# Kernel optimization log

Measured on AMD Instinct MI355X. Metric: run time of the kernel, lower is better.

## Reference

```python
import jax, jax.numpy as jnp
import numpy as np

B, S, HID = 2, 2048, 2048
NH, NKV, HD = 8, 2, 256
EPS = 1e-6
ROPE_THETA = 1e6


def _rms_norm(x, w):
    # Gemma3nRMSNorm: computed in fp32, x / sqrt(mean(x^2) + eps) * w
    xf = x.astype(jnp.float32)
    out = xf * jax.lax.rsqrt(jnp.mean(xf * xf, axis=-1, keepdims=True) + EPS) * w
    return out.astype(x.dtype)


def _rotate_half(x):
    x1, x2 = jnp.split(x, 2, axis=-1)
    return jnp.concatenate((-x2, x1), axis=-1)


def _apply_rope(x, cos, sin):
    # x: [B, S, H, D]; cos/sin: [B, S, D] -> unsqueeze head dim (unsqueeze_dim=2)
    c = cos[:, :, None, :]
    s = sin[:, :, None, :]
    return x * c + _rotate_half(x) * s


def setup_inputs() -> dict:
    key = jax.random.key(0)
    ks = jax.random.split(key, 6)
    hidden_states = jax.random.normal(ks[0], (B, S, HID), dtype=jnp.float32)
    # RoPE tables (theta = 1e6, Gemma3n)
    inv_freq = 1.0 / (ROPE_THETA ** (np.arange(0, HD, 2, dtype=np.float32) / HD))
    pos = np.arange(S, dtype=np.float32)
    freqs = pos[:, None] * inv_freq[None, :]            # [S, D/2]
    emb = np.concatenate([freqs, freqs], axis=-1)        # [S, D]
    cos = jnp.broadcast_to(jnp.asarray(np.cos(emb)), (B, S, HD)).astype(jnp.float32)
    sin = jnp.broadcast_to(jnp.asarray(np.sin(emb)), (B, S, HD)).astype(jnp.float32)
    # additive causal mask [B, 1, S, S]
    causal = jnp.tril(jnp.ones((S, S), dtype=bool))
    attention_mask = jnp.where(causal, 0.0, -1e9).astype(jnp.float32)
    attention_mask = jnp.broadcast_to(attention_mask[None, None], (B, 1, S, S))
    std = 0.02
    Wq = jax.random.normal(ks[1], (NH * HD, HID), dtype=jnp.float32) * std
    Wk = jax.random.normal(ks[2], (NKV * HD, HID), dtype=jnp.float32) * std
    Wv = jax.random.normal(ks[3], (NKV * HD, HID), dtype=jnp.float32) * std
    Wo = jax.random.normal(ks[4], (HID, NH * HD), dtype=jnp.float32) * std
    q_norm_w = jnp.ones((HD,), dtype=jnp.float32)
    k_norm_w = jnp.ones((HD,), dtype=jnp.float32)
    return {
        "hidden_states": hidden_states, "cos": cos, "sin": sin,
        "attention_mask": attention_mask,
        "Wq": Wq, "Wk": Wk, "Wv": Wv, "Wo": Wo,
        "q_norm_w": q_norm_w, "k_norm_w": k_norm_w,
    }


def reference(hidden_states, cos, sin, attention_mask, Wq, Wk, Wv, Wo, q_norm_w, k_norm_w):
    b, s, _ = hidden_states.shape
    # projections (no bias)
    q = (hidden_states @ Wq.T).reshape(b, s, NH, HD)
    k = (hidden_states @ Wk.T).reshape(b, s, NKV, HD)
    v = (hidden_states @ Wv.T).reshape(b, s, NKV, HD)
    # QK-norm then RoPE; v_norm has no scale (weight = 1)
    q = _apply_rope(_rms_norm(q, q_norm_w), cos, sin)
    k = _apply_rope(_rms_norm(k, k_norm_w), cos, sin)
    v = _rms_norm(v, jnp.float32(1.0))
    q = q.transpose(0, 2, 1, 3)  # [B, NH, S, D]
    k = k.transpose(0, 2, 1, 3)  # [B, NKV, S, D]
    v = v.transpose(0, 2, 1, 3)
    # repeat_kv: NKV -> NH (n_rep = NH // NKV)
    n_rep = NH // NKV
    k = jnp.repeat(k, n_rep, axis=1)
    v = jnp.repeat(v, n_rep, axis=1)
    # eager attention, scaling = 1.0 (as in Gemma3nTextAttention), no softcap
    scores = jnp.einsum("bhqd,bhkd->bhqk", q, k) + attention_mask
    probs = jax.nn.softmax(scores.astype(jnp.float32), axis=-1).astype(q.dtype)
    out = jnp.einsum("bhqk,bhkd->bqhd", probs, v).reshape(b, s, NH * HD)
    return out @ Wo.T
```

## Files before the change

kernel.cpp:

```cpp
#include <hip/hip_runtime.h>
#include <hip/hip_bf16.h>
#include <stdint.h>

#define S_LEN 2048
#define HIDN  2048
#define NH    8
#define NKV   2
#define HD    256

typedef _Float16 v8h __attribute__((ext_vector_type(8)));
typedef float    v4f __attribute__((ext_vector_type(4)));
typedef unsigned short u16;

struct alignas(8) US4 { u16 x, y, z, w; };

__device__ __forceinline__ u16 f2h(float f) {
  union { _Float16 h; u16 u; } t; t.h = (_Float16)f; return t.u;
}
__device__ __forceinline__ float h2f(u16 u) {
  union { _Float16 h; u16 u; } t; t.u = u; return (float)t.h;
}

template <typename T>
__device__ __forceinline__ void gload16(const T* g, void* l) {
  __builtin_amdgcn_global_load_lds(
      (const __attribute__((address_space(1))) void*)g,
      (__attribute__((address_space(3))) void*)l, 16, 0, 0);
}

__global__ void cvt_h_kernel(const float* __restrict__ in, u16* __restrict__ out, int n4) {
  int i = blockIdx.x * blockDim.x + threadIdx.x;
  if (i >= n4) return;
  float4 v = reinterpret_cast<const float4*>(in)[i];
  US4 o; o.x = f2h(v.x); o.y = f2h(v.y); o.z = f2h(v.z); o.w = f2h(v.w);
  reinterpret_cast<US4*>(out)[i] = o;
}

__global__ __launch_bounds__(256, 2) void gemm_h_nt(
    const u16* __restrict__ A, const u16* __restrict__ Bm,
    float* __restrict__ C, int M, int N, int K) {
  __shared__ u16 As[128 * 32];
  __shared__ u16 Bs[128 * 32];
  const int tid = threadIdx.x;
  const int w = tid >> 6, lane = tid & 63;
  const int m0 = blockIdx.x * 128, n0 = blockIdx.y * 128;
  const int wr = (w >> 1) * 64, wc = (w & 1) * 64;
  const int lr = lane & 15, lk = (lane >> 4) << 3;
  v4f acc[4][4] = {};
  const int row1 = tid >> 2, col1 = (tid & 3) << 3;
  const int t2 = tid + 256;
  const int row2 = t2 >> 2, col2 = (t2 & 3) << 3;
  for (int kt = 0; kt < K; kt += 32) {
    __syncthreads();
    gload16(A  + (size_t)(m0 + row1) * K + kt + col1, (char*)As + tid * 16);
    gload16(Bm + (size_t)(n0 + row1) * K + kt + col1, (char*)Bs + tid * 16);
    gload16(A  + (size_t)(m0 + row2) * K + kt + col2, (char*)As + t2 * 16);
    gload16(Bm + (size_t)(n0 + row2) * K + kt + col2, (char*)Bs + t2 * 16);
    __syncthreads();
    v8h af[4], bfr[4];
#pragma unroll
    for (int i = 0; i < 4; i++) af[i]  = *reinterpret_cast<const v8h*>(&As[(wr + i * 16 + lr) * 32 + lk]);
#pragma unroll
    for (int i = 0; i < 4; i++) bfr[i] = *reinterpret_cast<const v8h*>(&Bs[(wc + i * 16 + lr) * 32 + lk]);
#pragma unroll
    for (int i = 0; i < 4; i++)
#pragma unroll
      for (int jn = 0; jn < 4; jn++)
        acc[i][jn] = __builtin_amdgcn_mfma_f32_16x16x32_f16(af[i], bfr[jn], acc[i][jn], 0, 0, 0);
  }
  const int rbase = m0 + wr + ((lane >> 4) << 2);
  const int cbase = n0 + wc + lr;
#pragma unroll
  for (int i = 0; i < 4; i++)
#pragma unroll
    for (int jn = 0; jn < 4; jn++) {
      const int col = cbase + jn * 16;
#pragma unroll
      for (int j = 0; j < 4; j++)
        C[(size_t)(rbase + i * 16 + j) * N + col] = acc[i][jn][j];
    }
}

__global__ __launch_bounds__(256, 4) void norm_rope_kernel(
    const float* __restrict__ qkv, const float* __restrict__ cosb, const float* __restrict__ sinb,
    const float* __restrict__ qw, const float* __restrict__ kw,
    u16* __restrict__ q_t, u16* __restrict__ k_t, u16* __restrict__ v_t) {
  const int task = blockIdx.x * 4 + (threadIdx.x >> 6);
  const int lane = threadIdx.x & 63;
  const int unit = task % 12;
  const int ms = task / 12;
  const int b = ms >> 11, s = ms & 2047;
  const int d0 = lane << 2;
  const int col0 = (unit < 8) ? unit * 256 : 2048 + (unit - 8) * 256;
  const float4 xv = *reinterpret_cast<const float4*>(qkv + (size_t)ms * 3072 + col0 + d0);
  float x[4] = { xv.x, xv.y, xv.z, xv.w };
  float ss = x[0]*x[0] + x[1]*x[1] + x[2]*x[2] + x[3]*x[3];
#pragma unroll
  for (int m = 1; m < 64; m <<= 1) ss += __shfl_xor(ss, m, 64);
  const float r = rsqrtf(ss * (1.0f / 256.0f) + 1e-6f);
  if (unit < 10) {
    const float4 wv = *reinterpret_cast<const float4*>(((unit < 8) ? qw : kw) + d0);
    float xn[4];
    xn[0] = x[0] * r * wv.x; xn[1] = x[1] * r * wv.y;
    xn[2] = x[2] * r * wv.z; xn[3] = x[3] * r * wv.w;
    float rot[4];
#pragma unroll
    for (int j = 0; j < 4; j++) {
      const float p = __shfl(xn[j], lane ^ 32, 64);
      rot[j] = (lane < 32) ? -p : p;
    }
    const float4 c  = *reinterpret_cast<const float4*>(cosb + (size_t)ms * 256 + d0);
    const float4 sn = *reinterpret_cast<const float4*>(sinb + (size_t)ms * 256 + d0);
    US4 o;
    o.x = f2h(xn[0] * c.x + rot[0] * sn.x);
    o.y = f2h(xn[1] * c.y + rot[1] * sn.y);
    o.z = f2h(xn[2] * c.z + rot[2] * sn.z);
    o.w = f2h(xn[3] * c.w + rot[3] * sn.w);
    if (unit < 8) {
      const size_t dst = ((size_t)(b * NH + unit) * S_LEN + s) * 256 + d0;
      *reinterpret_cast<US4*>(q_t + dst) = o;
    } else {
      const size_t dst = ((size_t)(b * NKV + (unit - 8)) * S_LEN + s) * 256 + d0;
      *reinterpret_cast<US4*>(k_t + dst) = o;
    }
  } else {
    const int kvh = unit - 10;
    u16* vt = v_t + (size_t)(b * NKV + kvh) * 256 * 2048;
#pragma unroll
    for (int j = 0; j < 4; j++)
      vt[(size_t)(d0 + j) * 2048 + s] = f2h(x[j] * r);
  }
}

__device__ __forceinline__ void stage_tile(
    const u16* __restrict__ kb, const u16* __restrict__ vb, int kt,
    char* Ks, char* Vs, int tid) {
#pragma unroll
  for (int it = 0; it < 4; it++) {
    const int t = tid + it * 512;
    {
      const int slot = t & 3, kv = (t >> 2) & 63, ks = t >> 8;
      const int c8 = slot ^ ((kv >> 1) & 3);
      gload16(kb + (size_t)(kt * 64 + kv) * 256 + ks * 32 + c8 * 8, Ks + t * 16);
    }
    {
      const int slot = t & 3, d = (t >> 2) & 255, kss = t >> 10;
      const int c8 = slot ^ ((d >> 1) & 3);
      gload16(vb + (size_t)d * 2048 + kt * 64 + kss * 32 + c8 * 8, Vs + t * 16);
    }
  }
}

__global__ __launch_bounds__(512, 2) void attn_kernel(
    const u16* __restrict__ q_t, const u16* __restrict__ k_t,
    const u16* __restrict__ v_t, u16* __restrict__ aout) {
  const int qt = blockIdx.x;
  const int bh = blockIdx.y;
  const int b = bh >> 3, h = bh & 7, hk = h >> 2;
  const int tid = threadIdx.x;
  const int w = tid >> 6, lane = tid & 63;
  const int lr = lane & 15, ls = lane >> 4;

  __shared__ u16 KshB[2][8][64][32];
  __shared__ u16 VtsB[2][2][256][32];
  __shared__ u16 Ps[8][2][16][32];

  const u16* qb = q_t + ((size_t)(b * NH + h) * S_LEN + qt * 128 + w * 16) * 256;
  v8h qf[8];
#pragma unroll
  for (int f = 0; f < 8; f++)
    qf[f] = *reinterpret_cast<const v8h*>(qb + lr * 256 + f * 32 + ls * 8);

  v4f o[16] = {};
  float mr[4] = { -1e30f, -1e30f, -1e30f, -1e30f };
  float lsum[4] = {};

  const u16* kb = k_t + (size_t)(b * NKV + hk) * S_LEN * 256;
  const u16* vb = v_t + (size_t)(b * NKV + hk) * 256 * S_LEN;

  const int ntile = 2 * qt + 2;
  stage_tile(kb, vb, 0, (char*)KshB[0], (char*)VtsB[0], tid);

  for (int kt = 0; kt < ntile; kt++) {
    const int cb = kt & 1;
    if (kt + 1 < ntile) {
      stage_tile(kb, vb, kt + 1, (char*)KshB[cb ^ 1], (char*)VtsB[cb ^ 1], tid);
      asm volatile("s_waitcnt vmcnt(8)" ::: "memory");
    } else {
      asm volatile("s_waitcnt vmcnt(0)" ::: "memory");
    }
    __builtin_amdgcn_s_barrier();
    __builtin_amdgcn_sched_barrier(0);

    v4f sacc[4] = {};
#pragma unroll
    for (int ks = 0; ks < 8; ks++) {
#pragma unroll
      for (int n = 0; n < 4; n++) {
        const int row = n * 16 + lr;
        const v8h kf = *reinterpret_cast<const v8h*>(
            &KshB[cb][ks][row][(ls ^ ((row >> 1) & 3)) << 3]);
        sacc[n] = __builtin_amdgcn_mfma_f32_16x16x32_f16(qf[ks], kf, sacc[n], 0, 0, 0);
      }
    }
    if (kt >= 2 * qt) {
      const int rowg = qt * 128 + w * 16 + ls * 4;
#pragma unroll
      for (int n = 0; n < 4; n++) {
        const int colg = kt * 64 + n * 16 + lr;
#pragma unroll
        for (int j = 0; j < 4; j++)
          if (colg > rowg + j) sacc[n][j] = -1e30f;
      }
    }
    float pm[4];
#pragma unroll
    for (int j = 0; j < 4; j++)
      pm[j] = fmaxf(fmaxf(sacc[0][j], sacc[1][j]), fmaxf(sacc[2][j], sacc[3][j]));
#pragma unroll
    for (int m = 1; m < 16; m <<= 1)
#pragma unroll
      for (int j = 0; j < 4; j++) pm[j] = fmaxf(pm[j], __shfl_xor(pm[j], m, 64));
    float sc[4], rs[4];
#pragma unroll
    for (int j = 0; j < 4; j++) {
      const float mn = fmaxf(mr[j], pm[j]);
      sc[j] = __expf(mr[j] - mn);
      mr[j] = mn;
      rs[j] = 0.f;
    }
#pragma unroll
    for (int n = 0; n < 4; n++)
#pragma unroll
      for (int j = 0; j < 4; j++) {
        const float p = __expf(sacc[n][j] - mr[j]);
        rs[j] += p;
        const int row = ls * 4 + j;
        const int chi = (((n & 1) << 1) | (lr >> 3)) ^ ((row >> 1) & 3);
        Ps[w][n >> 1][row][chi * 8 + (lr & 7)] = f2h(p);
      }
#pragma unroll
    for (int m = 1; m < 16; m <<= 1)
#pragma unroll
      for (int j = 0; j < 4; j++) rs[j] += __shfl_xor(rs[j], m, 64);
#pragma unroll
    for (int j = 0; j < 4; j++) lsum[j] = lsum[j] * sc[j] + rs[j];
#pragma unroll
    for (int df = 0; df < 16; df++)
#pragma unroll
      for (int j = 0; j < 4; j++) o[df][j] *= sc[j];
#pragma unroll
    for (int kss = 0; kss < 2; kss++) {
      const v8h pa = *reinterpret_cast<const v8h*>(
          &Ps[w][kss][lr][(ls ^ ((lr >> 1) & 3)) << 3]);
#pragma unroll
      for (int df = 0; df < 16; df++) {
        const int d = df * 16 + lr;
        const v8h vf = *reinterpret_cast<const v8h*>(
            &VtsB[cb][kss][d][(ls ^ ((d >> 1) & 3)) << 3]);
        o[df] = __builtin_amdgcn_mfma_f32_16x16x32_f16(pa, vf, o[df], 0, 0, 0);
      }
    }
    __builtin_amdgcn_s_barrier();
  }

  float inv[4];
#pragma unroll
  for (int j = 0; j < 4; j++) inv[j] = 1.0f / lsum[j];
  u16* ob = aout + ((size_t)(b * 2048 + qt * 128 + w * 16 + ls * 4)) * 2048 + h * 256 + lr;
#pragma unroll
  for (int df = 0; df < 16; df++)
#pragma unroll
    for (int j = 0; j < 4; j++)
      ob[(size_t)j * 2048 + df * 16] = f2h(o[df][j] * inv[j]);
}

extern "C" void kernel_launch(void* const* d_in, const int* in_sizes, int n_in,
                              void* d_out, int out_size, void* d_ws, size_t ws_size,
                              hipStream_t stream) {
  const float* hs   = (const float*)d_in[0];
  const float* cosb = (const float*)d_in[1];
  const float* sinb = (const float*)d_in[2];
  const float* Wq = (const float*)d_in[4];
  const float* Wk = (const float*)d_in[5];
  const float* Wv = (const float*)d_in[6];
  const float* Wo = (const float*)d_in[7];
  const float* qw = (const float*)d_in[8];
  const float* kw = (const float*)d_in[9];
  float* out = (float*)d_out;

  char* ws = (char*)d_ws;
  u16* hs_f = (u16*)(ws + 0);
  u16* w_f  = (u16*)(ws + 16777216);
  u16* wo_f = (u16*)(ws + 29360128);
  float* qkv = (float*)(ws + 37748736);
  u16* q_t  = (u16*)(ws + 88080384);
  u16* k_t  = (u16*)(ws + 104857600);
  u16* v_t  = (u16*)(ws + 109051904);
  u16* aout = (u16*)(ws + 0);

  cvt_h_kernel<<<8192, 256, 0, stream>>>(hs, hs_f, 2097152);
  cvt_h_kernel<<<4096, 256, 0, stream>>>(Wq, w_f,           1048576);
  cvt_h_kernel<<<1024, 256, 0, stream>>>(Wk, w_f + 4194304, 262144);
  cvt_h_kernel<<<1024, 256, 0, stream>>>(Wv, w_f + 5242880, 262144);
  cvt_h_kernel<<<4096, 256, 0, stream>>>(Wo, wo_f,          1048576);

  gemm_h_nt<<<dim3(32, 24), 256, 0, stream>>>(hs_f, w_f, qkv, 4096, 3072, 2048);
  norm_rope_kernel<<<12288, 256, 0, stream>>>(qkv, cosb, sinb, qw, kw, q_t, k_t, v_t);
  attn_kernel<<<dim3(16, 16), 512, 0, stream>>>(q_t, k_t, v_t, aout);
  gemm_h_nt<<<dim3(32, 16), 256, 0, stream>>>(aout, wo_f, out, 4096, 2048, 2048);
}
```

Measured before the change: 273.0 us.

## Split-KV attention with 32x32 MFMA, register P, lazy rescale, combine kernel

Attention now splits each query tile's causal KV range into two halves across blocks, launched heaviest-first, and writes partial fp16 outputs plus per-row max and sum for a new combine kernel to merge. The inner loop moves to 32x32x16 MFMA with S computed transposed (K as A-operand), so P stays in registers and is repacked via lane shuffles instead of going through LDS. Online-softmax rescaling is skipped when the max grows by at most 8, and LDS swizzles are rewritten. The aim is better load balance and occupancy across CUs plus fewer LDS round-trips, at the cost of an extra kernel launch, partial-output traffic and fp16 rounding of the partial results.

```diff
diff --git a/kernel.cpp b/kernel.cpp
--- a/kernel.cpp
+++ b/kernel.cpp
@@ -8,8 +8,9 @@
 #define NKV   2
 #define HD    256
 
-typedef _Float16 v8h __attribute__((ext_vector_type(8)));
-typedef float    v4f __attribute__((ext_vector_type(4)));
+typedef _Float16 v8h  __attribute__((ext_vector_type(8)));
+typedef float    v4f  __attribute__((ext_vector_type(4)));
+typedef float    v16f __attribute__((ext_vector_type(16)));
 typedef unsigned short u16;
 
 struct alignas(8) US4 { u16 x, y, z, w; };
@@ -19,6 +20,9 @@
 }
 __device__ __forceinline__ float h2f(u16 u) {
   union { _Float16 h; u16 u; } t; t.u = u; return (float)t.h;
+}
+__device__ __forceinline__ uint32_t pk2(float a, float b) {
+  return (uint32_t)f2h(a) | ((uint32_t)f2h(b) << 16);
 }
 
 template <typename T>
@@ -132,59 +136,57 @@
   }
 }
 
-__device__ __forceinline__ void stage_tile(
+__device__ __forceinline__ void stage_kv(
     const u16* __restrict__ kb, const u16* __restrict__ vb, int kt,
-    char* Ks, char* Vs, int tid) {
+    u16* Kbuf, u16* Vbuf, int tid) {
 #pragma unroll
   for (int it = 0; it < 4; it++) {
-    const int t = tid + it * 512;
-    {
-      const int slot = t & 3, kv = (t >> 2) & 63, ks = t >> 8;
-      const int c8 = slot ^ ((kv >> 1) & 3);
-      gload16(kb + (size_t)(kt * 64 + kv) * 256 + ks * 32 + c8 * 8, Ks + t * 16);
-    }
-    {
-      const int slot = t & 3, d = (t >> 2) & 255, kss = t >> 10;
-      const int c8 = slot ^ ((d >> 1) & 3);
-      gload16(vb + (size_t)d * 2048 + kt * 64 + kss * 32 + c8 * 8, Vs + t * 16);
-    }
+    const int i1 = tid + it * 512;
+    const int kv = i1 >> 5, sp = i1 & 31;
+    const int sl = sp ^ (kv & 31);
+    gload16(kb + (size_t)(kt * 64 + kv) * 256 + sl * 8, (char*)Kbuf + i1 * 16);
+    const int d = i1 >> 3, sp2 = i1 & 7;
+    const int sl2 = sp2 ^ ((d >> 2) & 7);
+    gload16(vb + (size_t)d * 2048 + kt * 64 + sl2 * 8, (char*)Vbuf + i1 * 16);
   }
 }
 
 __global__ __launch_bounds__(512, 2) void attn_kernel(
     const u16* __restrict__ q_t, const u16* __restrict__ k_t,
-    const u16* __restrict__ v_t, u16* __restrict__ aout) {
-  const int qt = blockIdx.x;
+    const u16* __restrict__ v_t, u16* __restrict__ oP, float2* __restrict__ ml) {
+  const int qt = 15 - (blockIdx.x >> 1);
+  const int z  = blockIdx.x & 1;
   const int bh = blockIdx.y;
   const int b = bh >> 3, h = bh & 7, hk = h >> 2;
   const int tid = threadIdx.x;
   const int w = tid >> 6, lane = tid & 63;
-  const int lr = lane & 15, ls = lane >> 4;
-
-  __shared__ u16 KshB[2][8][64][32];
-  __shared__ u16 VtsB[2][2][256][32];
-  __shared__ u16 Ps[8][2][16][32];
-
-  const u16* qb = q_t + ((size_t)(b * NH + h) * S_LEN + qt * 128 + w * 16) * 256;
-  v8h qf[8];
-#pragma unroll
-  for (int f = 0; f < 8; f++)
-    qf[f] = *reinterpret_cast<const v8h*>(qb + lr * 256 + f * 32 + ls * 8);
-
-  v4f o[16] = {};
-  float mr[4] = { -1e30f, -1e30f, -1e30f, -1e30f };
-  float lsum[4] = {};
+  const int g = w >> 1, hf = w & 1;
+  const int l31 = lane & 31, hi = lane >> 5;
+
+  __shared__ u16 Kb[2][16384];
+  __shared__ u16 Vb[2][16384];
+
+  const u16* qb = q_t + ((size_t)(b * NH + h) * S_LEN + qt * 128 + g * 32 + l31) * 256;
+  v8h qf[16];
+#pragma unroll
+  for (int f = 0; f < 16; f++)
+    qf[f] = *reinterpret_cast<const v8h*>(qb + f * 16 + hi * 8);
+
+  v16f o[4] = {};
+  float mr = -1e30f, lsum = 0.f;
 
   const u16* kb = k_t + (size_t)(b * NKV + hk) * S_LEN * 256;
   const u16* vb = v_t + (size_t)(b * NKV + hk) * 256 * S_LEN;
 
-  const int ntile = 2 * qt + 2;
-  stage_tile(kb, vb, 0, (char*)KshB[0], (char*)VtsB[0], tid);
-
-  for (int kt = 0; kt < ntile; kt++) {
-    const int cb = kt & 1;
-    if (kt + 1 < ntile) {
-      stage_tile(kb, vb, kt + 1, (char*)KshB[cb ^ 1], (char*)VtsB[cb ^ 1], tid);
+  const int kt0 = z * (qt + 1);
+  const int kt1 = kt0 + (qt + 1);
+
+  stage_kv(kb, vb, kt0, Kb[0], Vb[0], tid);
+
+  for (int kt = kt0; kt < kt1; kt++) {
+    const int cb = (kt - kt0) & 1;
+    if (kt + 1 < kt1) {
+      stage_kv(kb, vb, kt + 1, Kb[cb ^ 1], Vb[cb ^ 1], tid);
       asm volatile("s_waitcnt vmcnt(8)" ::: "memory");
     } else {
       asm volatile("s_waitcnt vmcnt(0)" ::: "memory");
@@ -192,87 +194,125 @@
     __builtin_amdgcn_s_barrier();
     __builtin_amdgcn_sched_barrier(0);
 
-    v4f sacc[4] = {};
-#pragma unroll
-    for (int ks = 0; ks < 8; ks++) {
-#pragma unroll
-      for (int n = 0; n < 4; n++) {
-        const int row = n * 16 + lr;
-        const v8h kf = *reinterpret_cast<const v8h*>(
-            &KshB[cb][ks][row][(ls ^ ((row >> 1) & 3)) << 3]);
-        sacc[n] = __builtin_amdgcn_mfma_f32_16x16x32_f16(qf[ks], kf, sacc[n], 0, 0, 0);
+    v16f s0 = {}, s1 = {};
+#pragma unroll
+    for (int ds = 0; ds < 16; ds++) {
+      const int sp = (ds * 2 + hi) ^ l31;
+      const v8h kf0 = *reinterpret_cast<const v8h*>(&Kb[cb][l31 * 256 + sp * 8]);
+      const v8h kf1 = *reinterpret_cast<const v8h*>(&Kb[cb][(32 + l31) * 256 + sp * 8]);
+      s0 = __builtin_amdgcn_mfma_f32_32x32x16_f16(kf0, qf[ds], s0, 0, 0, 0);
+      s1 = __builtin_amdgcn_mfma_f32_32x32x16_f16(kf1, qf[ds], s1, 0, 0, 0);
+    }
+    if (kt >= 2 * qt) {
+      const int qg = qt * 128 + g * 32 + l31;
+#pragma unroll
+      for (int r = 0; r < 16; r++) {
+        const int kvr = kt * 64 + (r & 3) + 8 * (r >> 2) + 4 * hi;
+        if (kvr > qg) s0[r] = -1e30f;
+        if (kvr + 32 > qg) s1[r] = -1e30f;
       }
     }
-    if (kt >= 2 * qt) {
-      const int rowg = qt * 128 + w * 16 + ls * 4;
-#pragma unroll
-      for (int n = 0; n < 4; n++) {
-        const int colg = kt * 64 + n * 16 + lr;
-#pragma unroll
-        for (int j = 0; j < 4; j++)
-          if (colg > rowg + j) sacc[n][j] = -1e30f;
+    float pm = s0[0];
+#pragma unroll
+    for (int r = 1; r < 16; r++) pm = fmaxf(pm, s0[r]);
+#pragma unroll
+    for (int r = 0; r < 16; r++) pm = fmaxf(pm, s1[r]);
+    pm = fmaxf(pm, __shfl_xor(pm, 32, 64));
+    if (!__all(pm - mr <= 8.0f)) {
+      const float mn = fmaxf(mr, pm);
+      const float sc = __expf(mr - mn);
+      mr = mn;
+      lsum *= sc;
+#pragma unroll
+      for (int dblk = 0; dblk < 4; dblk++)
+#pragma unroll
+        for (int r = 0; r < 16; r++) o[dblk][r] *= sc;
+    }
+    float rs = 0.f;
+#pragma unroll
+    for (int r = 0; r < 16; r++) { s0[r] = __expf(s0[r] - mr); rs += s0[r]; }
+#pragma unroll
+    for (int r = 0; r < 16; r++) { s1[r] = __expf(s1[r] - mr); rs += s1[r]; }
+    rs += __shfl_xor(rs, 32, 64);
+    lsum += rs;
+    uint32_t pka[2][8], pkx[2][8];
+#pragma unroll
+    for (int u = 0; u < 8; u++) {
+      const int r = (u & 1) * 2 + (u >> 1) * 4;
+      pka[0][u] = pk2(s0[r], s0[r + 1]);
+      pka[1][u] = pk2(s1[r], s1[r + 1]);
+    }
+#pragma unroll
+    for (int n = 0; n < 2; n++)
+#pragma unroll
+      for (int u = 0; u < 8; u++)
+        pkx[n][u] = (uint32_t)__shfl_xor((int)pka[n][u], 32, 64);
+    v8h bfr[4];
+#pragma unroll
+    for (int s = 0; s < 4; s++) {
+      const int n = s >> 1, base = (s & 1) * 4;
+      union { uint32_t u[4]; v8h h; } t;
+      if (hi == 0) {
+        t.u[0] = pka[n][base];     t.u[1] = pka[n][base + 1];
+        t.u[2] = pkx[n][base];     t.u[3] = pkx[n][base + 1];
+      } else {
+        t.u[0] = pkx[n][base + 2]; t.u[1] = pkx[n][base + 3];
+        t.u[2] = pka[n][base + 2]; t.u[3] = pka[n][base + 3];
       }
-    }
-    float pm[4];
-#pragma unroll
-    for (int j = 0; j < 4; j++)
-      pm[j] = fmaxf(fmaxf(sacc[0][j], sacc[1][j]), fmaxf(sacc[2][j], sacc[3][j]));
-#pragma unroll
-    for (int m = 1; m < 16; m <<= 1)
-#pragma unroll
-      for (int j = 0; j < 4; j++) pm[j] = fmaxf(pm[j], __shfl_xor(pm[j], m, 64));
-    float sc[4], rs[4];
-#pragma unroll
-    for (int j = 0; j < 4; j++) {
-      const float mn = fmaxf(mr[j], pm[j]);
-      sc[j] = __expf(mr[j] - mn);
-      mr[j] = mn;
-      rs[j] = 0.f;
-    }
-#pragma unroll
-    for (int n = 0; n < 4; n++)
-#pragma unroll
-      for (int j = 0; j < 4; j++) {
-        const float p = __expf(sacc[n][j] - mr[j]);
-        rs[j] += p;
-        const int row = ls * 4 + j;
-        const int chi = (((n & 1) << 1) | (lr >> 3)) ^ ((row >> 1) & 3);
-        Ps[w][n >> 1][row][chi * 8 + (lr & 7)] = f2h(p);
+      bfr[s] = t.h;
+    }
+#pragma unroll
+    for (int dblk = 0; dblk < 4; dblk++) {
+      const int d = hf * 128 + dblk * 32 + l31;
+#pragma unroll
+      for (int s = 0; s < 4; s++) {
+        const int sp = (s * 2 + hi) ^ ((d >> 2) & 7);
+        const v8h vf = *reinterpret_cast<const v8h*>(&Vb[cb][d * 64 + sp * 8]);
+        o[dblk] = __builtin_amdgcn_mfma_f32_32x32x16_f16(vf, bfr[s], o[dblk], 0, 0, 0);
       }
-#pragma unroll
-    for (int m = 1; m < 16; m <<= 1)
-#pragma unroll
-      for (int j = 0; j < 4; j++) rs[j] += __shfl_xor(rs[j], m, 64);
-#pragma unroll
-    for (int j = 0; j < 4; j++) lsum[j] = lsum[j] * sc[j] + rs[j];
-#pragma unroll
-    for (int df = 0; df < 16; df++)
-#pragma unroll
-      for (int j = 0; j < 4; j++) o[df][j] *= sc[j];
-#pragma unroll
-    for (int kss = 0; kss < 2; kss++) {
-      const v8h pa = *reinterpret_cast<const v8h*>(
-          &Ps[w][kss][lr][(ls ^ ((lr >> 1) & 3)) << 3]);
-#pragma unroll
-      for (int df = 0; df < 16; df++) {
-        const int d = df * 16 + lr;
-        const v8h vf = *reinterpret_cast<const v8h*>(
-            &VtsB[cb][kss][d][(ls ^ ((d >> 1) & 3)) << 3]);
-        o[df] = __builtin_amdgcn_mfma_f32_16x16x32_f16(pa, vf, o[df], 0, 0, 0);
-      }
     }
     __builtin_amdgcn_s_barrier();
+    __builtin_amdgcn_sched_barrier(0);
   }
 
-  float inv[4];
-#pragma unroll
-  for (int j = 0; j < 4; j++) inv[j] = 1.0f / lsum[j];
-  u16* ob = aout + ((size_t)(b * 2048 + qt * 128 + w * 16 + ls * 4)) * 2048 + h * 256 + lr;
-#pragma unroll
-  for (int df = 0; df < 16; df++)
-#pragma unroll
-    for (int j = 0; j < 4; j++)
-      ob[(size_t)j * 2048 + df * 16] = f2h(o[df][j] * inv[j]);
+  const size_t rowi = (((size_t)(z * 16 + bh)) * 16 + qt) * 128 + g * 32 + l31;
+  u16* ob = oP + rowi * 256;
+#pragma unroll
+  for (int dblk = 0; dblk < 4; dblk++)
+#pragma unroll
+    for (int rr = 0; rr < 4; rr++) {
+      const int dbase = hf * 128 + dblk * 32 + rr * 8 + hi * 4;
+      uint2 pw;
+      pw.x = pk2(o[dblk][rr * 4 + 0], o[dblk][rr * 4 + 1]);
+      pw.y = pk2(o[dblk][rr * 4 + 2], o[dblk][rr * 4 + 3]);
+      *reinterpret_cast<uint2*>(ob + dbase) = pw;
+    }
+  if (hf == 0 && lane < 32)
+    ml[rowi] = make_float2(mr, lsum);
+}
+
+__global__ __launch_bounds__(256, 8) void combine_kernel(
+    const u16* __restrict__ oP, const float2* __restrict__ ml,
+    u16* __restrict__ aout) {
+  const int wid = threadIdx.x >> 6, lane = threadIdx.x & 63;
+  const int R = blockIdx.x * 4 + wid;
+  const int bh = R >> 11, rem = R & 2047, qt = rem >> 7, row = rem & 127;
+  const int b = bh >> 3, h = bh & 7;
+  const size_t i0 = (((size_t)bh)      * 16 + qt) * 128 + row;
+  const size_t i1 = (((size_t)(16+bh)) * 16 + qt) * 128 + row;
+  const float2 m0 = ml[i0], m1 = ml[i1];
+  const float ms = fmaxf(m0.x, m1.x);
+  const float f0 = __expf(m0.x - ms), f1 = __expf(m1.x - ms);
+  const float inv = 1.0f / (m0.y * f0 + m1.y * f1);
+  const US4 a = reinterpret_cast<const US4*>(oP + i0 * 256)[lane];
+  const US4 c = reinterpret_cast<const US4*>(oP + i1 * 256)[lane];
+  US4 o;
+  o.x = f2h((h2f(a.x) * f0 + h2f(c.x) * f1) * inv);
+  o.y = f2h((h2f(a.y) * f0 + h2f(c.y) * f1) * inv);
+  o.z = f2h((h2f(a.z) * f0 + h2f(c.z) * f1) * inv);
+  o.w = f2h((h2f(a.w) * f0 + h2f(c.w) * f1) * inv);
+  u16* dst = aout + ((size_t)(b * 2048 + qt * 128 + row)) * 2048 + h * 256 + lane * 4;
+  *reinterpret_cast<US4*>(dst) = o;
 }
 
 extern "C" void kernel_launch(void* const* d_in, const int* in_sizes, int n_in,
@@ -297,6 +337,8 @@
   u16* q_t  = (u16*)(ws + 88080384);
   u16* k_t  = (u16*)(ws + 104857600);
   u16* v_t  = (u16*)(ws + 109051904);
+  u16* oP   = (u16*)(ws + 37748736);
+  float2* mlp = (float2*)(ws + 71303168);
   u16* aout = (u16*)(ws + 0);
 
   cvt_h_kernel<<<8192, 256, 0, stream>>>(hs, hs_f, 2097152);
@@ -307,6 +349,7 @@
 
   gemm_h_nt<<<dim3(32, 24), 256, 0, stream>>>(hs_f, w_f, qkv, 4096, 3072, 2048);
   norm_rope_kernel<<<12288, 256, 0, stream>>>(qkv, cosb, sinb, qw, kw, q_t, k_t, v_t);
-  attn_kernel<<<dim3(16, 16), 512, 0, stream>>>(q_t, k_t, v_t, aout);
+  attn_kernel<<<dim3(32, 16), 512, 0, stream>>>(q_t, k_t, v_t, oP, mlp);
+  combine_kernel<<<8192, 256, 0, stream>>>(oP, mlp, aout);
   gemm_h_nt<<<dim3(32, 16), 256, 0, stream>>>(aout, wo_f, out, 4096, 2048, 2048);
 }
```

New measurement: 289.7 us. 6.1% more time.
